# Kernel tuning notes

Measured on AMD Instinct MI355X. Metric: run time of the kernel, lower is better.

## Reference

```python
import jax, jax.numpy as jnp
import numpy as np

LOW_RANK = 32      # low_rank_dim
N_CAND = 2048      # n_candidates
CHUNK = 128        # chunk_size
AUX_PCT = 0.2      # Settings.aux_loss_percent


def _normalize(x, eps=1e-12):
    # matches torch.nn.functional.normalize(p=2, dim=-1)
    n = jnp.linalg.norm(x, axis=-1, keepdims=True)
    return x / jnp.maximum(n, eps)


def setup_inputs() -> dict:
    key = jax.random.key(0)
    k1, k2, k3 = jax.random.split(key, 3)
    V, D, B, S = 50257, 1024, 4, 2048
    return {
        "hidden_states": jax.random.normal(k1, (B, S, D), jnp.float32),
        "embedding_weight": jax.random.normal(k2, (V, D), jnp.float32) * 0.02,
        "logit_scale": jnp.asarray(2.6592, jnp.float32),
        "target_ids": jax.random.randint(k3, (B, S), 0, V, dtype=jnp.int32),
    }


def reference(hidden_states, embedding_weight, logit_scale, target_ids):
    d = hidden_states.shape[-1]
    h = hidden_states.reshape(-1, d)            # [T, d]
    t = target_ids.reshape(-1)                  # [T]
    T = h.shape[0]
    n_chunks = T // CHUNK                       # T assumed divisible by CHUNK

    # no_grad low-rank table used only for candidate scan
    w_low_norm = jax.lax.stop_gradient(_normalize(embedding_weight[:, :LOW_RANK]))  # [V, L]
    h_low = _normalize(h[:, :LOW_RANK]).reshape(n_chunks, CHUNK, LOW_RANK)          # [n, C, L]
    h_full = _normalize(h).reshape(n_chunks, CHUNK, d)                              # [n, C, d]
    t_c = t.reshape(n_chunks, CHUNK)

    scale = 100.0 * jax.nn.sigmoid(logit_scale) + 1.0

    # with_batch_mean=True path: one scan per chunk using chunk-mean query (no_grad)
    h_mean = jax.lax.stop_gradient(h_low.mean(axis=1))      # [n, L]
    scan_logits = h_mean @ w_low_norm.T                     # [n, V]
    _, top_idx = jax.lax.top_k(scan_logits, N_CAND)         # [n, K]

    cand = embedding_weight[top_idx]                        # [n, K, d] (gather)
    cand_n = _normalize(cand)
    full_sims = jnp.einsum('ncd,nkd->nck', h_full, cand_n)  # [n, C, K]

    w_low_cand = _normalize(cand[..., :LOW_RANK])           # [n, K, L]
    low_sims = jnp.einsum('ncl,nkl->nck', h_low, w_low_cand)

    tgt_emb = embedding_weight[t_c]                         # [n, C, d]
    tgt_full_sim = jnp.sum(h_full * _normalize(tgt_emb), axis=-1)              # [n, C]
    tgt_low_sim = jnp.sum(h_low * _normalize(tgt_emb[..., :LOW_RANK]), axis=-1)

    is_tgt = top_idx[:, None, :] == t_c[:, :, None]         # [n, C, K]
    neg_inf = jnp.float32(-jnp.inf)

    # cross_entropy with label 0 == logsumexp(logits) - logits[..., 0]
    main_logits = jnp.concatenate(
        [tgt_full_sim[..., None] * scale,
         jnp.where(is_tgt, neg_inf, full_sims * scale)], axis=-1)
    main_loss = jnp.sum(jax.nn.logsumexp(main_logits, axis=-1) - main_logits[..., 0])

    aux_logits = jnp.concatenate(
        [tgt_low_sim[..., None] * scale,
         jnp.where(is_tgt, neg_inf, low_sims * scale)], axis=-1)
    aux_loss = jnp.sum(jax.nn.logsumexp(aux_logits, axis=-1) - aux_logits[..., 0])

    return (main_loss + AUX_PCT * aux_loss) / T
```

## Files before the change

kernel.cpp:

```cpp
#include <hip/hip_runtime.h>
#include <cstdint>
#include <cstddef>

#define V_SIZE 50257
#define V_PAD  50432
#define NV4    (V_PAD/4)
#define NVB    ((V_SIZE + 3) / 4)
#define D_DIM  1024
#define T_TOK  8192
#define NCHUNK 64
#define CCHUNK 128
#define NCAND  2048
#define NTILES 16
#define LOWR   32
#define SDCAP  6144
#define ESCALE 32.0f

typedef unsigned int  uint32;
typedef unsigned short u16;
typedef unsigned char u8;
typedef unsigned long long u64;
typedef __attribute__((ext_vector_type(8))) short short8;
typedef __attribute__((ext_vector_type(4))) float f32x4;

__device__ __forceinline__ u16 f2bf(float f){
  uint32 u = __float_as_uint(f);
  return (u16)((u + 0x7FFFu + ((u >> 16) & 1u)) >> 16);
}
__device__ __forceinline__ uint32 key_of(float f){
  uint32 b = __float_as_uint(f);
  return b ^ ((uint32)((int)b >> 31) | 0x80000000u);
}
__device__ __forceinline__ float sigscale(const float* lsc){
  return 100.f / (1.f + __expf(-lsc[0])) + 1.f;
}
__device__ __forceinline__ float wred_sum(float v){
  #pragma unroll
  for (int m = 32; m >= 1; m >>= 1) v += __shfl_xor(v, m, 64);
  return v;
}
__device__ __forceinline__ float wred_max(float v){
  #pragma unroll
  for (int m = 32; m >= 1; m >>= 1) v = fmaxf(v, __shfl_xor(v, m, 64));
  return v;
}
__device__ __forceinline__ void gload_lds16(const void* g, void* l){
  __builtin_amdgcn_global_load_lds(
      (const __attribute__((address_space(1))) uint32*)g,
      (__attribute__((address_space(3))) uint32*)l, 16, 0, 0);
}
__device__ __forceinline__ void load_row16(const float* base, int lane, float* f){
  const float4* s4 = (const float4*)(base + lane * 16);
  float4 t0 = s4[0], t1 = s4[1], t2 = s4[2], t3 = s4[3];
  f[0]=t0.x; f[1]=t0.y; f[2]=t0.z;  f[3]=t0.w;
  f[4]=t1.x; f[5]=t1.y; f[6]=t1.z;  f[7]=t1.w;
  f[8]=t2.x; f[9]=t2.y; f[10]=t2.z; f[11]=t2.w;
  f[12]=t3.x; f[13]=t3.y; f[14]=t3.z; f[15]=t3.w;
}
__device__ __forceinline__ void store_bf16x16(u16* dst_base, int lane, const float* f){
  uint32 pk[8];
  #pragma unroll
  for (int i=0;i<8;++i) pk[i] = (uint32)f2bf(f[2*i]) | ((uint32)f2bf(f[2*i+1]) << 16);
  uint4* d = (uint4*)(dst_base + lane * 16);
  d[0] = make_uint4(pk[0],pk[1],pk[2],pk[3]);
  d[1] = make_uint4(pk[4],pk[5],pk[6],pk[7]);
}
__device__ __forceinline__ void store_fp8x16(u8* dst_base, int lane, const float* f, float sc){
  uint32 pk[4];
  #pragma unroll
  for (int i=0;i<4;++i){
    int w = __builtin_amdgcn_cvt_pk_fp8_f32(f[4*i]*sc,   f[4*i+1]*sc, 0, false);
    w     = __builtin_amdgcn_cvt_pk_fp8_f32(f[4*i+2]*sc, f[4*i+3]*sc, w, true);
    pk[i] = (uint32)w;
  }
  *(uint4*)(dst_base + lane * 16) = make_uint4(pk[0],pk[1],pk[2],pk[3]);
}
__device__ __forceinline__ int a8(int r, int slot8){
  return r*64 + ((((slot8>>1) ^ (r&3))) << 4) + ((slot8&1) << 3);
}

__global__ void __launch_bounds__(256)
prep_kernel(const float* __restrict__ emb, u8* __restrict__ emb8,
            u16* __restrict__ elow16,
            float* __restrict__ invn_f, float* __restrict__ invn_l,
            float* __restrict__ wlow,
            const float* __restrict__ h, u8* __restrict__ h8,
            u16* __restrict__ hlow16,
            float* __restrict__ invh_f, float* __restrict__ invh_l,
            float* __restrict__ hpart, float* __restrict__ out)
{
  const int bid = blockIdx.x;
  const int tid = threadIdx.x, lane = tid & 63, wid = tid >> 6;
  if (bid < NVB){
    if (bid == 0 && tid == 0) out[0] = 0.f;
    const int v = bid * 4 + wid;
    if (v >= V_SIZE) return;
    float f[16];
    load_row16(emb + (size_t)v * D_DIM, lane, f);
    float ss = 0.f;
    #pragma unroll
    for (int k=0;k<16;++k) ss += f[k]*f[k];
    float fullss = wred_sum(ss);
    float lowss  = wred_sum(lane < 2 ? ss : 0.f);
    store_fp8x16(emb8 + (size_t)v * D_DIM, lane, f, ESCALE);
    if (lane < 2){
      store_bf16x16(elow16 + (size_t)v * LOWR, lane, f);
      float4* wp = (float4*)(wlow + (size_t)v * LOWR + lane * 16);
      wp[0] = make_float4(f[0], f[1], f[2],  f[3]);
      wp[1] = make_float4(f[4], f[5], f[6],  f[7]);
      wp[2] = make_float4(f[8], f[9], f[10], f[11]);
      wp[3] = make_float4(f[12],f[13],f[14], f[15]);
    }
    if (lane == 0){
      invn_f[v] = 1.f / fmaxf(sqrtf(fullss), 1e-12f);
      invn_l[v] = 1.f / fmaxf(sqrtf(lowss),  1e-12f);
    }
    return;
  }
  const int bid2 = bid - NVB;
  const int nchunk = bid2 >> 3, sub = bid2 & 7;
  __shared__ float hm[LOWR];
  if (tid < LOWR) hm[tid] = 0.f;
  __syncthreads();
  for (int i = 0; i < 4; ++i){
    const int loc = sub*16 + wid*4 + i;
    const int tok = nchunk * CCHUNK + loc;
    float f[16];
    load_row16(h + (size_t)tok * D_DIM, lane, f);
    float ss = 0.f;
    #pragma unroll
    for (int k=0;k<16;++k) ss += f[k]*f[k];
    float fullss = wred_sum(ss);
    float lowss  = wred_sum(lane < 2 ? ss : 0.f);
    float invf = 1.f / fmaxf(sqrtf(fullss), 1e-12f);
    float invl = 1.f / fmaxf(sqrtf(lowss),  1e-12f);
    store_fp8x16(h8 + (size_t)tok * D_DIM, lane, f, 1.0f);
    if (lane < 2) store_bf16x16(hlow16 + (size_t)tok * LOWR, lane, f);
    if (lane == 0){ invh_f[tok] = invf; invh_l[tok] = invl; }
    if (lane < 2){
      #pragma unroll
      for (int k=0;k<16;++k) atomicAdd(&hm[lane*16 + k], f[k] * invl * (1.f/128.f));
    }
  }
  __syncthreads();
  if (tid < LOWR) hpart[(size_t)(nchunk*8 + sub) * LOWR + tid] = hm[tid];
}

__global__ void __launch_bounds__(256)
scan_kernel(const float* __restrict__ wlow, const float* __restrict__ invn_l,
            const float* __restrict__ hpart, float* __restrict__ scan)
{
  __shared__ float hm[NCHUNK * LOWR];
  for (int i = threadIdx.x; i < NCHUNK * LOWR; i += 256){
    const int nn = i >> 5, l = i & 31;
    float s = 0.f;
    #pragma unroll
    for (int p = 0; p < 8; ++p) s += hpart[(size_t)(nn*8 + p) * LOWR + l];
    hm[i] = s;
  }
  __syncthreads();
  const int v = blockIdx.x * 256 + threadIdx.x;
  if (v >= V_SIZE){
    if (v < V_PAD)
      for (int nn = 0; nn < NCHUNK; ++nn) scan[(size_t)nn * V_PAD + v] = -3.4e38f;
    return;
  }
  float w[LOWR];
  const float4* s4 = (const float4*)(wlow + (size_t)v * LOWR);
  #pragma unroll
  for (int i=0;i<8;++i){
    float4 t = s4[i];
    w[4*i]=t.x; w[4*i+1]=t.y; w[4*i+2]=t.z; w[4*i+3]=t.w;
  }
  const float inv = invn_l[v];
  #pragma unroll
  for (int i=0;i<LOWR;++i) w[i] *= inv;
  for (int nn = 0; nn < NCHUNK; ++nn){
    float d = 0.f;
    #pragma unroll
    for (int l=0;l<LOWR;++l) d += w[l] * hm[nn*LOWR + l];
    scan[(size_t)nn * V_PAD + v] = d;
  }
}

__global__ void __launch_bounds__(1024)
topk_all(const float* __restrict__ scan,
         const float* __restrict__ invn_f, const float* __restrict__ invn_l,
         int* __restrict__ topidx, float* __restrict__ invc_f, float* __restrict__ invc_l)
{
  const int nchunk = blockIdx.x, tid = threadIdx.x, lane = tid & 63;
  __shared__ uint32 h8v[8][2048];
  __shared__ int gt_list[2048];
  __shared__ u64 sd_list[SDCAP];
  __shared__ uint32 rh[256];
  __shared__ uint32 n_gt, n_sd, s_tb, s_cgt, s_sel, s_cum, s_pos;
  if (tid == 0){ n_gt = 0; n_sd = 0; s_pos = 0; }
  for (int i = tid; i < 8*2048; i += 1024) (&h8v[0][0])[i] = 0;
  __syncthreads();
  const float4* row = (const float4*)(scan + (size_t)nchunk * V_PAD);
  const int cp = (tid >> 6) & 7;
  for (int i = tid; i < NV4; i += 1024){
    float4 x = row[i];
    atomicAdd(&h8v[cp][key_of(x.x) >> 21], 1u);
    atomicAdd(&h8v[cp][key_of(x.y) >> 21], 1u);
    atomicAdd(&h8v[cp][key_of(x.z) >> 21], 1u);
    atomicAdd(&h8v[cp][key_of(x.w) >> 21], 1u);
  }
  __syncthreads();
  for (int i = tid; i < 2048; i += 1024){
    uint32 s = h8v[0][i];
    #pragma unroll
    for (int c = 1; c < 8; ++c) s += h8v[c][i];
    h8v[0][i] = s;
  }
  __syncthreads();
  if (tid < 64){
    uint32 c = 0;
    #pragma unroll 8
    for (int k = 0; k < 32; ++k) c += h8v[0][lane*32 + k];
    uint32 s = c;
    #pragma unroll
    for (int off = 1; off < 64; off <<= 1){
      uint32 t = __shfl_down(s, off, 64);
      if (lane + off < 64) s += t;
    }
    u64 m1 = __ballot(s >= NCAND);
    const int g = 63 - __builtin_clzll(m1);
    const uint32 cum = (g < 63) ? __shfl(s, g + 1, 64) : 0u;
    uint32 s2 = (lane < 32) ? h8v[0][g*32 + lane] : 0u;
    #pragma unroll
    for (int off = 1; off < 32; off <<= 1){
      uint32 t = __shfl_down(s2, off, 64);
      if (lane + off < 32) s2 += t;
    }
    u64 m2 = __ballot((lane < 32) && (cum + s2 >= NCAND));
    const int j = 63 - __builtin_clzll(m2);
    const uint32 cgt = cum + ((j < 31) ? __shfl(s2, j + 1, 64) : 0u);
    if (lane == 0){ s_tb = (uint32)(g*32 + j); s_cgt = cgt; }
  }
  __syncthreads();
  const uint32 tb = s_tb, cgt = s_cgt;
  for (int i = tid; i < NV4; i += 1024){
    float4 x = row[i];
    const int vbase = i * 4;
    float vals[4] = {x.x, x.y, x.z, x.w};
    #pragma unroll
    for (int c = 0; c < 4; ++c){
      uint32 u = key_of(vals[c]);
      uint32 b = u >> 21;
      const int v = vbase + c;
      const bool ok = (v < V_SIZE) && (b >= tb);
      const bool is_gt = ok && (b > tb);
      const bool is_sd = ok && (b == tb);
      const u64 mg = __ballot(is_gt);
      if (mg){
        const int ldr = (int)__builtin_ctzll(mg);
        uint32 base = 0;
        if (lane == ldr) base = atomicAdd(&n_gt, (uint32)__popcll(mg));
        base = __shfl(base, ldr, 64);
        if (is_gt){
          uint32 p = base + (uint32)__popcll(mg & ((1ull << lane) - 1ull));
          if (p < 2048u) gt_list[p] = v;
        }
      }
      const u64 ms = __ballot(is_sd);
      if (ms){
        const int ldr = (int)__builtin_ctzll(ms);
        uint32 base = 0;
        if (lane == ldr) base = atomicAdd(&n_sd, (uint32)__popcll(ms));
        base = __shfl(base, ldr, 64);
        if (is_sd){
          uint32 p = base + (uint32)__popcll(ms & ((1ull << lane) - 1ull));
          if (p < (uint32)SDCAP) sd_list[p] = ((u64)(~u) << 32) | (uint32)v;
        }
      }
    }
  }
  __syncthreads();
  const uint32 ng = n_gt < 2048u ? n_gt : 2048u;
  for (uint32 i = tid; i < ng; i += 1024){
    const int v = gt_list[i];
    const int o = nchunk * NCAND + (int)i;
    topidx[o] = v; invc_f[o] = invn_f[v]; invc_l[o] = invn_l[v];
  }
  const int n = (int)(n_sd < (uint32)SDCAP ? n_sd : (uint32)SDCAP);
  uint32 r = NCAND - cgt; if ((int)r > n) r = (uint32)n;
  u64 pref = sd_list[0] & 0xFF00000000000000ull;
  uint32 rem = r;
  const int bytes6[6] = {6,5,4,2,1,0};
  for (int bi = 0; bi < 6; ++bi){
    const int by = bytes6[bi];
    if (tid < 256) rh[tid] = 0;
    __syncthreads();
    const u64 pmask = (~0ull) << ((by+1)*8);
    for (int i = tid; i < n; i += 1024){
      u64 x = sd_list[i];
      if ((x & pmask) == pref) atomicAdd(&rh[(uint32)(x >> (by*8)) & 255u], 1u);
    }
    __syncthreads();
    if (tid < 64){
      const uint32 b0 = rh[lane*4], b1 = rh[lane*4+1], b2 = rh[lane*4+2], b3 = rh[lane*4+3];
      uint32 ps = b0 + b1 + b2 + b3;
      #pragma unroll
      for (int off = 1; off < 64; off <<= 1){
        uint32 t = __shfl_up(ps, off, 64);
        if (lane >= off) ps += t;
      }
      const u64 mm = __ballot(ps >= rem);
      const int gl = (int)__builtin_ctzll(mm);
      const uint32 before = (gl > 0) ? __shfl(ps, gl-1, 64) : 0u;
      if (lane == gl){
        uint32 cum = before; uint32 bsel = (uint32)gl * 4;
        if (cum + b0 < rem){ cum += b0; bsel++;
          if (cum + b1 < rem){ cum += b1; bsel++;
            if (cum + b2 < rem){ cum += b2; bsel++; } } }
        s_sel = bsel; s_cum = cum;
      }
    }
    __syncthreads();
    pref |= ((u64)s_sel) << (by*8);
    rem -= s_cum;
    __syncthreads();
  }
  for (int i = tid; i < n; i += 1024){
    u64 x = sd_list[i];
    if (x <= pref){
      uint32 p = atomicAdd(&s_pos, 1u);
      const int v = (int)(uint32)x;
      const int o = nchunk * NCAND + (int)(cgt + p);
      topidx[o] = v; invc_f[o] = invn_f[v]; invc_l[o] = invn_l[v];
    }
  }
}

__global__ void __launch_bounds__(256)
gemm_fused(const u8* __restrict__ h8, const u8* __restrict__ emb8,
           const u16* __restrict__ hlow16, const u16* __restrict__ elow16,
           const int* __restrict__ topidx,
           const float* __restrict__ invh_f, const float* __restrict__ invc_f,
           const float* __restrict__ invh_l, const float* __restrict__ invc_l,
           const int* __restrict__ tgts, const float* __restrict__ lsc,
           float* __restrict__ pm, float* __restrict__ pa)
{
  constexpr int NSTEP = 16;
  const int id = blockIdx.x;
  const int s_ = id >> 3;
  const int ntile = s_ & 15;
  const int nchunk = ((s_ >> 4) << 3) | (id & 7);
  const int tid = threadIdx.x, lane = tid & 63, wid = tid >> 6;
  const int wm = wid >> 1, wn = wid & 1;
  const int fq = lane >> 4, fr = lane & 15;

  __shared__ u8 As[CCHUNK * 64];
  __shared__ u8 Bs[CCHUNK * 64];
  __shared__ float s_invh[CCHUNK], s_invc[CCHUNK];
  __shared__ float s_invhl[CCHUNK], s_invcl[CCHUNK];
  __shared__ int   s_tgt[CCHUNK], s_idx[CCHUNK];

  if (tid < CCHUNK){
    s_invh[tid]  = invh_f[nchunk * CCHUNK + tid];
    s_invhl[tid] = invh_l[nchunk * CCHUNK + tid];
    s_tgt[tid]   = tgts[nchunk * CCHUNK + tid];
    int o = nchunk * NCAND + ntile * CCHUNK + tid;
    s_idx[tid]   = topidx[o];
    s_invc[tid]  = invc_f[o];
    s_invcl[tid] = invc_l[o];
  }

  const int rl = lane >> 2;
  const int cbyte = ((lane & 3) ^ (rl & 3)) * 16;
  const char* aptr[2];
  const char* bptr[2];
  #pragma unroll
  for (int s = 0; s < 2; ++s){
    int row = wid * 32 + s * 16 + rl;
    aptr[s] = (const char*)h8 + ((size_t)(nchunk * CCHUNK + row)) * D_DIM + cbyte;
    int cidx = topidx[nchunk * NCAND + ntile * CCHUNK + row];
    bptr[s] = (const char*)emb8 + (size_t)cidx * D_DIM + cbyte;
  }

  f32x4 acc[4][4];
  #pragma unroll
  for (int m=0;m<4;++m)
    #pragma unroll
    for (int q=0;q<4;++q)
      acc[m][q] = (f32x4){0.f,0.f,0.f,0.f};

  for (int st = 0; st < NSTEP; ++st){
    const int koff = st * 64;
    #pragma unroll
    for (int s = 0; s < 2; ++s){
      gload_lds16(aptr[s] + koff, (void*)&As[(wid*32 + s*16) * 64]);
      gload_lds16(bptr[s] + koff, (void*)&Bs[(wid*32 + s*16) * 64]);
    }
    __syncthreads();
    #pragma unroll
    for (int kk = 0; kk < 2; ++kk){
      long af[4], bf[4];
      #pragma unroll
      for (int m=0;m<4;++m)
        af[m] = *(const long*)&As[a8(wm*64 + m*16 + fr, kk*4 + fq)];
      #pragma unroll
      for (int q=0;q<4;++q)
        bf[q] = *(const long*)&Bs[a8(wn*64 + q*16 + fr, kk*4 + fq)];
      #pragma unroll
      for (int m=0;m<4;++m)
        #pragma unroll
        for (int q=0;q<4;++q)
          acc[m][q] = __builtin_amdgcn_mfma_f32_16x16x32_fp8_fp8(af[m], bf[q], acc[m][q], 0, 0, 0);
    }
    __syncthreads();
  }

  {
    #pragma unroll
    for (int s = 0; s < 2; ++s){
      int row = wid * 32 + s * 16 + rl;
      const char* ap = (const char*)hlow16 + ((size_t)(nchunk * CCHUNK + row)) * (LOWR*2) + cbyte;
      int cidx = topidx[nchunk * NCAND + ntile * CCHUNK + row];
      const char* bp = (const char*)elow16 + (size_t)cidx * (LOWR*2) + cbyte;
      gload_lds16(ap, (void*)&As[(wid*32 + s*16) * 64]);
      gload_lds16(bp, (void*)&Bs[(wid*32 + s*16) * 64]);
    }
  }

  const float scale = sigscale(lsc);
  const float scm = scale * (1.0f / ESCALE);
  const float NEG = -__builtin_huge_valf();

  #pragma unroll
  for (int m=0;m<4;++m){
    #pragma unroll
    for (int j=0;j<4;++j){
      const int c = wm*64 + m*16 + fq*4 + j;
      const float ihs = s_invh[c] * scm;
      const int tg = s_tgt[c];
      float vals[4];
      #pragma unroll
      for (int q=0;q<4;++q){
        const int kl = wn*64 + q*16 + fr;
        float lg = acc[m][q][j] * ihs * s_invc[kl];
        vals[q] = (s_idx[kl] == tg) ? NEG : lg;
      }
      float lmax = fmaxf(fmaxf(vals[0], vals[1]), fmaxf(vals[2], vals[3]));
      #pragma unroll
      for (int ms=1; ms<16; ms<<=1) lmax = fmaxf(lmax, __shfl_xor(lmax, ms, 64));
      float se = 0.f;
      #pragma unroll
      for (int q=0;q<4;++q) se += __expf(vals[q] - lmax);
      #pragma unroll
      for (int ms=1; ms<16; ms<<=1) se += __shfl_xor(se, ms, 64);
      if (fr == 0){
        size_t pos = ((size_t)((nchunk*NTILES + ntile)*2 + wn) * CCHUNK + c) * 2;
        pm[pos]   = lmax;
        pm[pos+1] = se;
      }
    }
  }

  __syncthreads();

  f32x4 acc2[4][4];
  {
    short8 afa[4], bfa[4];
    #pragma unroll
    for (int m=0;m<4;++m){
      const int r = wm*64 + m*16 + fr;
      afa[m] = *(const short8*)&As[r*64 + ((fq ^ (r & 3)) << 4)];
    }
    #pragma unroll
    for (int q=0;q<4;++q){
      const int r = wn*64 + q*16 + fr;
      bfa[q] = *(const short8*)&Bs[r*64 + ((fq ^ (r & 3)) << 4)];
    }
    #pragma unroll
    for (int m=0;m<4;++m)
      #pragma unroll
      for (int q=0;q<4;++q)
        acc2[m][q] = __builtin_amdgcn_mfma_f32_16x16x32_bf16(
            afa[m], bfa[q], (f32x4){0.f,0.f,0.f,0.f}, 0, 0, 0);
  }

  #pragma unroll
  for (int m=0;m<4;++m){
    #pragma unroll
    for (int j=0;j<4;++j){
      const int c = wm*64 + m*16 + fq*4 + j;
      const float ihs = s_invhl[c] * scale;
      const int tg = s_tgt[c];
      float vals[4];
      #pragma unroll
      for (int q=0;q<4;++q){
        const int kl = wn*64 + q*16 + fr;
        float lg = acc2[m][q][j] * ihs * s_invcl[kl];
        vals[q] = (s_idx[kl] == tg) ? NEG : lg;
      }
      float lmax = fmaxf(fmaxf(vals[0], vals[1]), fmaxf(vals[2], vals[3]));
      #pragma unroll
      for (int ms=1; ms<16; ms<<=1) lmax = fmaxf(lmax, __shfl_xor(lmax, ms, 64));
      float se = 0.f;
      #pragma unroll
      for (int q=0;q<4;++q) se += __expf(vals[q] - lmax);
      #pragma unroll
      for (int ms=1; ms<16; ms<<=1) se += __shfl_xor(se, ms, 64);
      if (fr == 0){
        size_t pos = ((size_t)((nchunk*NTILES + ntile)*2 + wn) * CCHUNK + c) * 2;
        pa[pos]   = lmax;
        pa[pos+1] = se;
      }
    }
  }
}

__global__ void __launch_bounds__(256)
merge_loss(const float* __restrict__ h, const float* __restrict__ emb,
           const int* __restrict__ tgts,
           const float* __restrict__ invh_f, const float* __restrict__ invh_l,
           const float* __restrict__ invn_f, const float* __restrict__ invn_l,
           const float* __restrict__ pm, const float* __restrict__ pa,
           const float* __restrict__ lsc, float* __restrict__ out)
{
  const int nchunk = blockIdx.x >> 2, quarter = blockIdx.x & 3;
  const int tid = threadIdx.x, lane = tid & 63, wid = tid >> 6;
  const float scale = sigscale(lsc);
  const float NEG = -__builtin_huge_valf();
  float wacc = 0.f;
  for (int i = 0; i < 8; ++i){
    const int loc = quarter*32 + wid*8 + i;
    const int tok = nchunk * CCHUNK + loc;
    const int t = tgts[tok];
    float hf[16], ef[16];
    load_row16(h + (size_t)tok * D_DIM, lane, hf);
    load_row16(emb + (size_t)t * D_DIM, lane, ef);
    float part = 0.f;
    #pragma unroll
    for (int k=0;k<16;++k) part += hf[k]*ef[k];
    float dfull = wred_sum(part);
    float dlow  = wred_sum(lane < 2 ? part : 0.f);
    float tful = dfull * invh_f[tok] * invn_f[t] * scale;
    float tlow = dlow  * invh_l[tok] * invn_l[t] * scale;

    float mi = NEG, si = 0.f, mia = NEG, sia = 0.f;
    if (lane < 32){
      size_t q = ((size_t)(nchunk*32 + lane) * CCHUNK + loc) * 2;
      mi  = pm[q]; si  = pm[q+1];
      mia = pa[q]; sia = pa[q+1];
    }
    float M  = wred_max(mi);
    float S  = wred_sum(lane < 32 ? si * __expf(mi - M) : 0.f);
    float M2 = fmaxf(M, tful);
    float lmain = __logf(S * __expf(M - M2) + __expf(tful - M2)) + M2 - tful;
    float Ma  = wred_max(mia);
    float Sa  = wred_sum(lane < 32 ? sia * __expf(mia - Ma) : 0.f);
    float M2a = fmaxf(Ma, tlow);
    float laux = __logf(Sa * __expf(Ma - M2a) + __expf(tlow - M2a)) + M2a - tlow;
    wacc += lmain + 0.2f * laux;
  }
  __shared__ float ws4[4];
  if (lane == 0) ws4[wid] = wacc;
  __syncthreads();
  if (tid == 0) atomicAdd(out, (ws4[0]+ws4[1]+ws4[2]+ws4[3]) * (1.f / (float)T_TOK));
}

extern "C" void kernel_launch(void* const* d_in, const int* in_sizes, int n_in,
                              void* d_out, int out_size, void* d_ws, size_t ws_size,
                              hipStream_t stream)
{
  (void)in_sizes; (void)n_in; (void)out_size; (void)ws_size;
  const float* h   = (const float*)d_in[0];
  const float* emb = (const float*)d_in[1];
  const float* lsc = (const float*)d_in[2];
  const int*   tgt = (const int*)d_in[3];
  float* out = (float*)d_out;

  uint8_t* p = (uint8_t*)d_ws;
  auto carve = [&](size_t n)->uint8_t*{
    uint8_t* r = p; p += (n + 255) & ~(size_t)255; return r;
  };
  u8*    emb8   = (u8*)   carve((size_t)V_SIZE * D_DIM);
  u16*   elow16 = (u16*)  carve((size_t)V_SIZE * LOWR * 2);
  float* invn_f = (float*)carve((size_t)V_SIZE * 4);
  float* invn_l = (float*)carve((size_t)V_SIZE * 4);
  float* wlow   = (float*)carve((size_t)V_SIZE * LOWR * 4);
  u8*    h8     = (u8*)   carve((size_t)T_TOK * D_DIM);
  u16*   hlow16 = (u16*)  carve((size_t)T_TOK * LOWR * 2);
  float* invh_f = (float*)carve((size_t)T_TOK * 4);
  float* invh_l = (float*)carve((size_t)T_TOK * 4);
  float* hpart  = (float*)carve((size_t)NCHUNK * 8 * LOWR * 4);
  float* scan   = (float*)carve((size_t)NCHUNK * V_PAD * 4);
  int*   topidx = (int*)  carve((size_t)NCHUNK * NCAND * 4);
  float* invc_f = (float*)carve((size_t)NCHUNK * NCAND * 4);
  float* invc_l = (float*)carve((size_t)NCHUNK * NCAND * 4);
  float* pm     = (float*)carve((size_t)NCHUNK * 32 * CCHUNK * 2 * 4);
  float* pa     = (float*)carve((size_t)NCHUNK * 32 * CCHUNK * 2 * 4);

  prep_kernel<<<dim3(NVB + NCHUNK*8), dim3(256), 0, stream>>>(
      emb, emb8, elow16, invn_f, invn_l, wlow, h, h8, hlow16, invh_f, invh_l, hpart, out);
  scan_kernel<<<dim3(V_PAD / 256), dim3(256), 0, stream>>>(wlow, invn_l, hpart, scan);
  topk_all<<<dim3(NCHUNK), dim3(1024), 0, stream>>>(
      scan, invn_f, invn_l, topidx, invc_f, invc_l);
  gemm_fused<<<dim3(NTILES * NCHUNK), dim3(256), 0, stream>>>(
      h8, emb8, hlow16, elow16, topidx, invh_f, invc_f, invh_l, invc_l, tgt, lsc, pm, pa);
  merge_loss<<<dim3(NCHUNK * 4), dim3(256), 0, stream>>>(
      h, emb, tgt, invh_f, invh_l, invn_f, invn_l, pm, pa, lsc, out);
}
```

Baseline: 192.1 us.

## Double-buffer LDS tiles in fused candidate GEMM to overlap loads with MFMA

```diff
diff --git a/kernel.cpp b/kernel.cpp
--- a/kernel.cpp
+++ b/kernel.cpp
@@ -351,8 +351,8 @@
   const int wm = wid >> 1, wn = wid & 1;
   const int fq = lane >> 4, fr = lane & 15;
 
-  __shared__ u8 As[CCHUNK * 64];
-  __shared__ u8 Bs[CCHUNK * 64];
+  __shared__ u8 As[2][CCHUNK * 64];
+  __shared__ u8 Bs[2][CCHUNK * 64];
   __shared__ float s_invh[CCHUNK], s_invc[CCHUNK];
   __shared__ float s_invhl[CCHUNK], s_invcl[CCHUNK];
   __shared__ int   s_tgt[CCHUNK], s_idx[CCHUNK];
@@ -371,13 +371,18 @@
   const int cbyte = ((lane & 3) ^ (rl & 3)) * 16;
   const char* aptr[2];
   const char* bptr[2];
+  const char* alptr[2];
+  const char* blptr[2];
   #pragma unroll
   for (int s = 0; s < 2; ++s){
     int row = wid * 32 + s * 16 + rl;
     aptr[s] = (const char*)h8 + ((size_t)(nchunk * CCHUNK + row)) * D_DIM + cbyte;
     int cidx = topidx[nchunk * NCAND + ntile * CCHUNK + row];
     bptr[s] = (const char*)emb8 + (size_t)cidx * D_DIM + cbyte;
-  }
+    alptr[s] = (const char*)hlow16 + ((size_t)(nchunk * CCHUNK + row)) * (LOWR*2) + cbyte;
+    blptr[s] = (const char*)elow16 + (size_t)cidx * (LOWR*2) + cbyte;
+  }
+  const int ldst = (wid*32 + rl) * 64;
 
   f32x4 acc[4][4];
   #pragma unroll
@@ -386,23 +391,38 @@
     for (int q=0;q<4;++q)
       acc[m][q] = (f32x4){0.f,0.f,0.f,0.f};
 
+  #pragma unroll
+  for (int s = 0; s < 2; ++s){
+    gload_lds16(aptr[s], (void*)&As[0][ldst + s*16*64]);
+    gload_lds16(bptr[s], (void*)&Bs[0][ldst + s*16*64]);
+  }
+  __syncthreads();
+
+  int cur = 0;
   for (int st = 0; st < NSTEP; ++st){
-    const int koff = st * 64;
-    #pragma unroll
-    for (int s = 0; s < 2; ++s){
-      gload_lds16(aptr[s] + koff, (void*)&As[(wid*32 + s*16) * 64]);
-      gload_lds16(bptr[s] + koff, (void*)&Bs[(wid*32 + s*16) * 64]);
-    }
-    __syncthreads();
+    if (st + 1 < NSTEP){
+      const int koff = (st + 1) * 64;
+      #pragma unroll
+      for (int s = 0; s < 2; ++s){
+        gload_lds16(aptr[s] + koff, (void*)&As[cur^1][ldst + s*16*64]);
+        gload_lds16(bptr[s] + koff, (void*)&Bs[cur^1][ldst + s*16*64]);
+      }
+    } else {
+      #pragma unroll
+      for (int s = 0; s < 2; ++s){
+        gload_lds16(alptr[s], (void*)&As[cur^1][ldst + s*16*64]);
+        gload_lds16(blptr[s], (void*)&Bs[cur^1][ldst + s*16*64]);
+      }
+    }
     #pragma unroll
     for (int kk = 0; kk < 2; ++kk){
       long af[4], bf[4];
       #pragma unroll
       for (int m=0;m<4;++m)
-        af[m] = *(const long*)&As[a8(wm*64 + m*16 + fr, kk*4 + fq)];
+        af[m] = *(const long*)&As[cur][a8(wm*64 + m*16 + fr, kk*4 + fq)];
       #pragma unroll
       for (int q=0;q<4;++q)
-        bf[q] = *(const long*)&Bs[a8(wn*64 + q*16 + fr, kk*4 + fq)];
+        bf[q] = *(const long*)&Bs[cur][a8(wn*64 + q*16 + fr, kk*4 + fq)];
       #pragma unroll
       for (int m=0;m<4;++m)
         #pragma unroll
@@ -410,18 +430,7 @@
           acc[m][q] = __builtin_amdgcn_mfma_f32_16x16x32_fp8_fp8(af[m], bf[q], acc[m][q], 0, 0, 0);
     }
     __syncthreads();
-  }
-
-  {
-    #pragma unroll
-    for (int s = 0; s < 2; ++s){
-      int row = wid * 32 + s * 16 + rl;
-      const char* ap = (const char*)hlow16 + ((size_t)(nchunk * CCHUNK + row)) * (LOWR*2) + cbyte;
-      int cidx = topidx[nchunk * NCAND + ntile * CCHUNK + row];
-      const char* bp = (const char*)elow16 + (size_t)cidx * (LOWR*2) + cbyte;
-      gload_lds16(ap, (void*)&As[(wid*32 + s*16) * 64]);
-      gload_lds16(bp, (void*)&Bs[(wid*32 + s*16) * 64]);
-    }
+    cur ^= 1;
   }
 
   const float scale = sigscale(lsc);
@@ -458,20 +467,18 @@
     }
   }
 
-  __syncthreads();
-
   f32x4 acc2[4][4];
   {
     short8 afa[4], bfa[4];
     #pragma unroll
     for (int m=0;m<4;++m){
       const int r = wm*64 + m*16 + fr;
-      afa[m] = *(const short8*)&As[r*64 + ((fq ^ (r & 3)) << 4)];
+      afa[m] = *(const short8*)&As[cur][r*64 + ((fq ^ (r & 3)) << 4)];
     }
     #pragma unroll
     for (int q=0;q<4;++q){
       const int r = wn*64 + q*16 + fr;
-      bfa[q] = *(const short8*)&Bs[r*64 + ((fq ^ (r & 3)) << 4)];
+      bfa[q] = *(const short8*)&Bs[cur][r*64 + ((fq ^ (r & 3)) << 4)];
     }
     #pragma unroll
     for (int m=0;m<4;++m)
```

After: 193.8 us. About the same (+0.9%).
